# Kernel tuning notes

Hardware: AMD Instinct MI355X
Metric: run time of the kernel (lower is better)

The kernel has to match this reference:

```python
import jax, jax.numpy as jnp
import numpy as np

B, I, H = 4096, 1024, 2048
NUM_STEPS = 5
DT = 0.1

def setup_inputs() -> dict:
    key = jax.random.key(0)
    ks = jax.random.split(key, 5)
    # xavier-normal-ish scales for weights
    return {
        "x": jax.random.normal(ks[0], (B, I), jnp.float32),
        "hidden": jax.random.normal(ks[1], (B, H), jnp.float32),
        "W_rec": jax.random.normal(ks[2], (H, H), jnp.float32) * (2.0 / (H + H)) ** 0.5,
        "W_in_w": jax.random.normal(ks[3], (H, I), jnp.float32) * (2.0 / (I + H)) ** 0.5,
        "W_in_b": jnp.zeros((H,), jnp.float32),
        "tau_base": jnp.ones((H,), jnp.float32) * 2.0,
        "tau_adapt_w": jax.random.normal(ks[4], (H, I + H), jnp.float32) * (2.0 / (I + 2 * H)) ** 0.5,
        "tau_adapt_b": jnp.zeros((H,), jnp.float32),
    }

def reference(x, hidden, W_rec, W_in_w, W_in_b, tau_base, tau_adapt_w, tau_adapt_b):
    # x: [B, I], hidden: [B, H]
    input_contrib = x @ W_in_w.T + W_in_b          # loop-invariant: [B, H]
    x_tau = x @ tau_adapt_w[:, :I].T               # loop-invariant part of tau_adapt
    h = hidden
    tau = None
    for _ in range(NUM_STEPS):
        # tau_adapt(cat[x, h]) split into x-part + h-part (same math as concat matmul)
        tau_logits = x_tau + h @ tau_adapt_w[:, I:].T + tau_adapt_b
        tau = tau_base * (0.5 + jax.nn.sigmoid(tau_logits))   # [B, H]
        activated = jnp.tanh(h @ W_rec.T + input_contrib)     # [B, H]
        h = h + DT * (-h + activated) / tau
    return (h, tau)
```

## Files before the change

kernel.cpp:

```cpp
#include <hip/hip_runtime.h>
#include <hip/hip_bf16.h>

#define B_DIM 4096
#define I_DIM 1024
#define H_DIM 2048

typedef __attribute__((ext_vector_type(4))) float f32x4;
typedef __attribute__((ext_vector_type(8))) __bf16 bf16x8;

static __device__ __forceinline__ unsigned short f2bf(float f) {
  unsigned int u = __builtin_bit_cast(unsigned int, f);
  u += 0x7fffu + ((u >> 16) & 1u);
  return (unsigned short)(u >> 16);
}
static __device__ __forceinline__ float bf2f(unsigned short u) {
  unsigned int v = (unsigned int)u << 16;
  return __builtin_bit_cast(float, v);
}

__global__ void cvt_f32_bf16(const float* __restrict__ src,
                             unsigned short* __restrict__ dst,
                             int total4, int cols4, int src_ld4, int col04) {
  int t = blockIdx.x * blockDim.x + threadIdx.x;
  if (t >= total4) return;
  int row = t / cols4;
  int c = t - row * cols4;
  float4 v = reinterpret_cast<const float4*>(src)[(size_t)row * src_ld4 + col04 + c];
  ushort4 o;
  o.x = f2bf(v.x); o.y = f2bf(v.y); o.z = f2bf(v.z); o.w = f2bf(v.w);
  reinterpret_cast<ushort4*>(dst)[t] = o;
}

__global__ void cvt_ilv_bf16(const float* __restrict__ src,
                             unsigned short* __restrict__ dst,
                             int total4, int cols4, int src_ld4, int col04, int which) {
  int t = blockIdx.x * blockDim.x + threadIdx.x;
  if (t >= total4) return;
  int srow = t / cols4;
  int c = t - srow * cols4;
  int drow = ((srow >> 4) << 5) + (srow & 15) + which * 16;
  float4 v = reinterpret_cast<const float4*>(src)[(size_t)srow * src_ld4 + col04 + c];
  ushort4 o;
  o.x = f2bf(v.x); o.y = f2bf(v.y); o.z = f2bf(v.z); o.w = f2bf(v.w);
  reinterpret_cast<ushort4*>(dst)[(size_t)drow * cols4 + c] = o;
}

#define GLOAD_LDS16(gp, lp)                                                     \
  __builtin_amdgcn_global_load_lds(                                             \
      (const __attribute__((address_space(1))) void*)(gp),                      \
      (__attribute__((address_space(3))) void*)(lp), 16, 0, 0)

static __device__ __forceinline__ bf16x8 ldfrag(const unsigned short* p, int row, int l16) {
  return *reinterpret_cast<const bf16x8*>(p + row * 32 + ((l16 ^ ((row >> 1) & 3)) << 3));
}

template<int K, int MODE, bool WRITE_TAU>
__global__ __launch_bounds__(512, 2)
void gemm256(const unsigned short* __restrict__ Ab,
             const unsigned short* __restrict__ Wb,
             const unsigned short* __restrict__ add1b,
             const unsigned short* __restrict__ add2b,
             const float* __restrict__ wb,
             const float* __restrict__ tau_base,
             const float* __restrict__ tau_bias,
             const float* hprev,
             float* __restrict__ out1,
             float* out2,
             unsigned short* __restrict__ ob1,
             unsigned short* __restrict__ ob2) {
  __shared__ __align__(16) unsigned short lds[49152];

  const int tid  = threadIdx.x;
  const int lane = tid & 63;
  const int wid  = tid >> 6;
  const int wm   = wid >> 2;
  const int wn   = wid & 3;
  const int lr   = lane & 15;
  const int l16  = lane >> 4;

  const int bid = blockIdx.x;
  const int swz = (bid & 7) * 32 + (bid >> 3);
  const int bm = swz >> 4;
  const int bn = swz & 15;

  const unsigned short* Ag = Ab + (size_t)bm * 256 * K;
  const unsigned short* Wg = Wb + (size_t)bn * 256 * K;

  constexpr int NT = K / 32;

#define STAGE_OP(gcol, ldsbase)                                              \
  {                                                                          \
    { int s = tid;                                                           \
      int row = s >> 2;                                                      \
      int k16 = (s & 3) ^ ((row >> 1) & 3);                                  \
      GLOAD_LDS16((gcol) + (size_t)row * K + (k16 << 3),                     \
                  lds + (ldsbase) + s * 8); }                                \
    { int s = 512 + tid;                                                     \
      int row = s >> 2;                                                      \
      int k16 = (s & 3) ^ ((row >> 1) & 3);                                  \
      GLOAD_LDS16((gcol) + (size_t)row * K + (k16 << 3),                     \
                  lds + (ldsbase) + s * 8); }                                \
  }

  STAGE_OP(Ag, 0);
  STAGE_OP(Wg, 8192);
  STAGE_OP(Ag + 32, 16384);
  STAGE_OP(Wg + 32, 16384 + 8192);
  asm volatile("s_waitcnt vmcnt(4)" ::: "memory");
  __builtin_amdgcn_s_barrier();

  f32x4 acc[8][4];
  const f32x4 fz = {0.f, 0.f, 0.f, 0.f};
  #pragma unroll
  for (int i = 0; i < 8; ++i)
    #pragma unroll
    for (int j = 0; j < 4; ++j) acc[i][j] = fz;

  bf16x8 afr[4], bfr[4];
  int cb = 0;
  for (int t = 0; t < NT; ++t) {
    int nb = cb + 32768; if (nb >= 49152) nb -= 49152;
    const unsigned short* Acur = lds + cb;
    const unsigned short* Bcur = lds + cb + 8192;

    #pragma unroll
    for (int i = 0; i < 4; ++i) afr[i] = ldfrag(Acur, wm * 128 + i * 16 + lr, l16);
    #pragma unroll
    for (int j = 0; j < 4; ++j) bfr[j] = ldfrag(Bcur, wn * 64 + j * 16 + lr, l16);
    if (t + 2 < NT) { STAGE_OP(Ag + (size_t)(t + 2) * 32, nb); }
    asm volatile("" ::: "memory");
    __builtin_amdgcn_s_barrier();
    __builtin_amdgcn_s_setprio(1);
    #pragma unroll
    for (int i = 0; i < 4; ++i)
      #pragma unroll
      for (int j = 0; j < 4; ++j)
        acc[i][j] = __builtin_amdgcn_mfma_f32_16x16x32_bf16(afr[i], bfr[j], acc[i][j], 0, 0, 0);
    __builtin_amdgcn_s_setprio(0);
    __builtin_amdgcn_s_barrier();

    #pragma unroll
    for (int i = 0; i < 4; ++i) afr[i] = ldfrag(Acur, wm * 128 + (i + 4) * 16 + lr, l16);
    if (t + 2 < NT) { STAGE_OP(Wg + (size_t)(t + 2) * 32, nb + 8192); }
    asm volatile("" ::: "memory");
    if (t + 2 < NT)      { asm volatile("s_waitcnt vmcnt(4)" ::: "memory"); }
    else if (t + 1 < NT) { asm volatile("s_waitcnt vmcnt(0)" ::: "memory"); }
    __builtin_amdgcn_s_barrier();
    __builtin_amdgcn_s_setprio(1);
    #pragma unroll
    for (int i = 0; i < 4; ++i)
      #pragma unroll
      for (int j = 0; j < 4; ++j)
        acc[i + 4][j] = __builtin_amdgcn_mfma_f32_16x16x32_bf16(afr[i], bfr[j], acc[i + 4][j], 0, 0, 0);
    __builtin_amdgcn_s_setprio(0);
    __builtin_amdgcn_s_barrier();

    cb += 16384; if (cb >= 49152) cb = 0;
  }
#undef STAGE_OP

  const int rowg0 = bm * 256 + wm * 128 + l16 * 4;
  const int hcb = bn * 128 + wn * 32;
  #pragma unroll
  for (int p = 0; p < 2; ++p) {
    const int hc = hcb + p * 16 + lr;
    float tb = 0.f, tbi = 0.f, wbv = 0.f;
    if constexpr (MODE == 1) { tb = tau_base[hc]; tbi = tau_bias[hc]; }
    else                     { wbv = wb[hc]; }
    #pragma unroll
    for (int i = 0; i < 8; ++i) {
      const f32x4 c1 = acc[i][2 * p];
      const f32x4 c2 = acc[i][2 * p + 1];
      #pragma unroll
      for (int r = 0; r < 4; ++r) {
        const int row = rowg0 + i * 16 + r;
        const size_t idx = (size_t)row * H_DIM + hc;
        if constexpr (MODE == 0) {
          ob1[idx] = f2bf(c1[r] + wbv);
          ob2[idx] = f2bf(c2[r]);
        } else {
          const float hp  = hprev[idx];
          const float tl  = bf2f(add1b[idx]) + c1[r] + tbi;
          const float tau = tb * (0.5f + 1.f / (1.f + __expf(-tl)));
          const float pre = c2[r] + bf2f(add2b[idx]);
          const float act = 1.f - 2.f / (1.f + __expf(2.f * pre));
          const float hn  = hp + 0.1f * (act - hp) / tau;
          out1[idx] = hn;
          ob1[idx] = f2bf(hn);
          if constexpr (WRITE_TAU) out2[idx] = tau;
        }
      }
    }
  }
}

extern "C" void kernel_launch(void* const* d_in, const int* in_sizes, int n_in,
                              void* d_out, int out_size, void* d_ws, size_t ws_size,
                              hipStream_t stream) {
  const float* x           = (const float*)d_in[0];
  const float* hidden      = (const float*)d_in[1];
  const float* W_rec       = (const float*)d_in[2];
  const float* W_in_w      = (const float*)d_in[3];
  const float* W_in_b      = (const float*)d_in[4];
  const float* tau_base    = (const float*)d_in[5];
  const float* tau_adapt_w = (const float*)d_in[6];
  const float* tau_adapt_b = (const float*)d_in[7];

  float* out_h   = (float*)d_out;
  float* out_tau = (float*)d_out + (size_t)B_DIM * H_DIM;

  char* ws = (char*)d_ws;
  if (ws_size < 100663296u) return;
  unsigned short* x_bf   = (unsigned short*)(ws);
  unsigned short* hA_bf  = (unsigned short*)(ws +  8388608);
  unsigned short* hB_bf  = (unsigned short*)(ws + 25165824);
  unsigned short* Wpre   = (unsigned short*)(ws + 41943040);
  unsigned short* Wcat   = (unsigned short*)(ws + 50331648);
  unsigned short* icb    = (unsigned short*)(ws + 67108864);
  unsigned short* xtaub  = (unsigned short*)(ws + 83886080);

  cvt_f32_bf16<<<4096, 256, 0, stream>>>(x,      x_bf,  1048576, 256, 256, 0);
  cvt_f32_bf16<<<8192, 256, 0, stream>>>(hidden, hA_bf, 2097152, 512, 512, 0);
  cvt_ilv_bf16<<<2048, 256, 0, stream>>>(W_in_w,      Wpre, 524288, 256, 256, 0, 0);
  cvt_ilv_bf16<<<2048, 256, 0, stream>>>(tau_adapt_w, Wpre, 524288, 256, 768, 0, 1);
  cvt_ilv_bf16<<<4096, 256, 0, stream>>>(tau_adapt_w, Wcat, 1048576, 512, 768, 256, 0);
  cvt_ilv_bf16<<<4096, 256, 0, stream>>>(W_rec,       Wcat, 1048576, 512, 512, 0,   1);

  gemm256<1024, 0, false><<<256, 512, 0, stream>>>(
      x_bf, Wpre, nullptr, nullptr, W_in_b, nullptr, nullptr, nullptr,
      nullptr, nullptr, icb, xtaub);

  gemm256<2048, 1, false><<<256, 512, 0, stream>>>(
      hA_bf, Wcat, xtaub, icb, nullptr, tau_base, tau_adapt_b, hidden,
      out_h, nullptr, hB_bf, nullptr);
  gemm256<2048, 1, false><<<256, 512, 0, stream>>>(
      hB_bf, Wcat, xtaub, icb, nullptr, tau_base, tau_adapt_b, out_h,
      out_tau, nullptr, hA_bf, nullptr);
  gemm256<2048, 1, false><<<256, 512, 0, stream>>>(
      hA_bf, Wcat, xtaub, icb, nullptr, tau_base, tau_adapt_b, out_tau,
      out_h, nullptr, hB_bf, nullptr);
  gemm256<2048, 1, false><<<256, 512, 0, stream>>>(
      hB_bf, Wcat, xtaub, icb, nullptr, tau_base, tau_adapt_b, out_h,
      out_tau, nullptr, hA_bf, nullptr);
  gemm256<2048, 1, true><<<256, 512, 0, stream>>>(
      hA_bf, Wcat, xtaub, icb, nullptr, tau_base, tau_adapt_b, out_tau,
      out_h, out_tau, hB_bf, nullptr);
}
```

Baseline: 786.8 us.

## Shrink GEMM tile to 128x256 and launch 512 blocks for better CU fill

The GEMM tile shrinks from 256x256 to 128x256 rows per block. That halves the accumulator registers and the LDS footprint, raises the launch bound to 4 blocks per CU, and doubles the grid to 512 blocks so the 256 CUs are better filled. The k-loop is restructured to issue the A and B stage loads together with one barrier phase per k-step instead of two half-steps. The cost is lower arithmetic intensity per block and more re-reads of the weight tiles from L2.

```diff
diff --git a/kernel.cpp b/kernel.cpp
--- a/kernel.cpp
+++ b/kernel.cpp
@@ -55,20 +55,20 @@
 }
 
 template<int K, int MODE, bool WRITE_TAU>
-__global__ __launch_bounds__(512, 2)
-void gemm256(const unsigned short* __restrict__ Ab,
-             const unsigned short* __restrict__ Wb,
-             const unsigned short* __restrict__ add1b,
-             const unsigned short* __restrict__ add2b,
-             const float* __restrict__ wb,
-             const float* __restrict__ tau_base,
-             const float* __restrict__ tau_bias,
-             const float* hprev,
-             float* __restrict__ out1,
-             float* out2,
-             unsigned short* __restrict__ ob1,
-             unsigned short* __restrict__ ob2) {
-  __shared__ __align__(16) unsigned short lds[49152];
+__global__ __launch_bounds__(512, 4)
+void gemm128x256(const unsigned short* __restrict__ Ab,
+                 const unsigned short* __restrict__ Wb,
+                 const unsigned short* __restrict__ add1b,
+                 const unsigned short* __restrict__ add2b,
+                 const float* __restrict__ wb,
+                 const float* __restrict__ tau_base,
+                 const float* __restrict__ tau_bias,
+                 const float* hprev,
+                 float* __restrict__ out1,
+                 float* out2,
+                 unsigned short* __restrict__ ob1,
+                 unsigned short* __restrict__ ob2) {
+  __shared__ __align__(16) unsigned short lds[36864];
 
   const int tid  = threadIdx.x;
   const int lane = tid & 63;
@@ -79,57 +79,62 @@
   const int l16  = lane >> 4;
 
   const int bid = blockIdx.x;
-  const int swz = (bid & 7) * 32 + (bid >> 3);
-  const int bm = swz >> 4;
-  const int bn = swz & 15;
-
-  const unsigned short* Ag = Ab + (size_t)bm * 256 * K;
+  const int swz = (bid & 7) * 64 + (bid >> 3);
+  const int bn = swz >> 5;
+  const int bm = swz & 31;
+
+  const unsigned short* Ag = Ab + (size_t)bm * 128 * K;
   const unsigned short* Wg = Wb + (size_t)bn * 256 * K;
 
   constexpr int NT = K / 32;
 
-#define STAGE_OP(gcol, ldsbase)                                              \
-  {                                                                          \
-    { int s = tid;                                                           \
-      int row = s >> 2;                                                      \
+#define STAGE_A(gcol, base)                                                  \
+  { int s = tid; int row = s >> 2; int k16 = (s & 3) ^ ((row >> 1) & 3);     \
+    GLOAD_LDS16((gcol) + (size_t)row * K + (k16 << 3),                       \
+                lds + (base) + s * 8); }
+#define STAGE_B(gcol, base)                                                  \
+  { { int s = tid; int row = s >> 2; int k16 = (s & 3) ^ ((row >> 1) & 3);   \
+      GLOAD_LDS16((gcol) + (size_t)row * K + (k16 << 3),                     \
+                  lds + (base) + 4096 + s * 8); }                            \
+    { int s = 512 + tid; int row = s >> 2;                                   \
       int k16 = (s & 3) ^ ((row >> 1) & 3);                                  \
       GLOAD_LDS16((gcol) + (size_t)row * K + (k16 << 3),                     \
-                  lds + (ldsbase) + s * 8); }                                \
-    { int s = 512 + tid;                                                     \
-      int row = s >> 2;                                                      \
-      int k16 = (s & 3) ^ ((row >> 1) & 3);                                  \
-      GLOAD_LDS16((gcol) + (size_t)row * K + (k16 << 3),                     \
-                  lds + (ldsbase) + s * 8); }                                \
-  }
-
-  STAGE_OP(Ag, 0);
-  STAGE_OP(Wg, 8192);
-  STAGE_OP(Ag + 32, 16384);
-  STAGE_OP(Wg + 32, 16384 + 8192);
-  asm volatile("s_waitcnt vmcnt(4)" ::: "memory");
+                  lds + (base) + 4096 + s * 8); } }
+
+  STAGE_A(Ag, 0);
+  STAGE_B(Wg, 0);
+  STAGE_A(Ag + 32, 12288);
+  STAGE_B(Wg + 32, 12288);
+  asm volatile("s_waitcnt vmcnt(3)" ::: "memory");
   __builtin_amdgcn_s_barrier();
 
-  f32x4 acc[8][4];
+  f32x4 acc[4][4];
   const f32x4 fz = {0.f, 0.f, 0.f, 0.f};
   #pragma unroll
-  for (int i = 0; i < 8; ++i)
+  for (int i = 0; i < 4; ++i)
     #pragma unroll
     for (int j = 0; j < 4; ++j) acc[i][j] = fz;
 
-  bf16x8 afr[4], bfr[4];
   int cb = 0;
   for (int t = 0; t < NT; ++t) {
-    int nb = cb + 32768; if (nb >= 49152) nb -= 49152;
+    int nb = cb + 24576; if (nb >= 36864) nb -= 36864;
     const unsigned short* Acur = lds + cb;
-    const unsigned short* Bcur = lds + cb + 8192;
-
-    #pragma unroll
-    for (int i = 0; i < 4; ++i) afr[i] = ldfrag(Acur, wm * 128 + i * 16 + lr, l16);
+    const unsigned short* Bcur = lds + cb + 4096;
+
+    bf16x8 afr[4], bfr[4];
+    #pragma unroll
+    for (int i = 0; i < 4; ++i) afr[i] = ldfrag(Acur, wm * 64 + i * 16 + lr, l16);
     #pragma unroll
     for (int j = 0; j < 4; ++j) bfr[j] = ldfrag(Bcur, wn * 64 + j * 16 + lr, l16);
-    if (t + 2 < NT) { STAGE_OP(Ag + (size_t)(t + 2) * 32, nb); }
-    asm volatile("" ::: "memory");
-    __builtin_amdgcn_s_barrier();
+
+    if (t + 2 < NT) {
+      STAGE_A(Ag + (size_t)(t + 2) * 32, nb);
+      STAGE_B(Wg + (size_t)(t + 2) * 32, nb);
+      asm volatile("s_waitcnt vmcnt(3)" ::: "memory");
+    } else if (t + 1 < NT) {
+      asm volatile("s_waitcnt vmcnt(0)" ::: "memory");
+    }
+
     __builtin_amdgcn_s_setprio(1);
     #pragma unroll
     for (int i = 0; i < 4; ++i)
@@ -139,27 +144,12 @@
     __builtin_amdgcn_s_setprio(0);
     __builtin_amdgcn_s_barrier();
 
-    #pragma unroll
-    for (int i = 0; i < 4; ++i) afr[i] = ldfrag(Acur, wm * 128 + (i + 4) * 16 + lr, l16);
-    if (t + 2 < NT) { STAGE_OP(Wg + (size_t)(t + 2) * 32, nb + 8192); }
-    asm volatile("" ::: "memory");
-    if (t + 2 < NT)      { asm volatile("s_waitcnt vmcnt(4)" ::: "memory"); }
-    else if (t + 1 < NT) { asm volatile("s_waitcnt vmcnt(0)" ::: "memory"); }
-    __builtin_amdgcn_s_barrier();
-    __builtin_amdgcn_s_setprio(1);
-    #pragma unroll
-    for (int i = 0; i < 4; ++i)
-      #pragma unroll
-      for (int j = 0; j < 4; ++j)
-        acc[i + 4][j] = __builtin_amdgcn_mfma_f32_16x16x32_bf16(afr[i], bfr[j], acc[i + 4][j], 0, 0, 0);
-    __builtin_amdgcn_s_setprio(0);
-    __builtin_amdgcn_s_barrier();
-
-    cb += 16384; if (cb >= 49152) cb = 0;
+    cb += 12288; if (cb >= 36864) cb = 0;
   }
-#undef STAGE_OP
-
-  const int rowg0 = bm * 256 + wm * 128 + l16 * 4;
+#undef STAGE_A
+#undef STAGE_B
+
+  const int rowg0 = bm * 128 + wm * 64 + l16 * 4;
   const int hcb = bn * 128 + wn * 32;
   #pragma unroll
   for (int p = 0; p < 2; ++p) {
@@ -168,7 +158,7 @@
     if constexpr (MODE == 1) { tb = tau_base[hc]; tbi = tau_bias[hc]; }
     else                     { wbv = wb[hc]; }
     #pragma unroll
-    for (int i = 0; i < 8; ++i) {
+    for (int i = 0; i < 4; ++i) {
       const f32x4 c1 = acc[i][2 * p];
       const f32x4 c2 = acc[i][2 * p + 1];
       #pragma unroll
@@ -226,23 +216,23 @@
   cvt_ilv_bf16<<<4096, 256, 0, stream>>>(tau_adapt_w, Wcat, 1048576, 512, 768, 256, 0);
   cvt_ilv_bf16<<<4096, 256, 0, stream>>>(W_rec,       Wcat, 1048576, 512, 512, 0,   1);
 
-  gemm256<1024, 0, false><<<256, 512, 0, stream>>>(
+  gemm128x256<1024, 0, false><<<512, 512, 0, stream>>>(
       x_bf, Wpre, nullptr, nullptr, W_in_b, nullptr, nullptr, nullptr,
       nullptr, nullptr, icb, xtaub);
 
-  gemm256<2048, 1, false><<<256, 512, 0, stream>>>(
+  gemm128x256<2048, 1, false><<<512, 512, 0, stream>>>(
       hA_bf, Wcat, xtaub, icb, nullptr, tau_base, tau_adapt_b, hidden,
       out_h, nullptr, hB_bf, nullptr);
-  gemm256<2048, 1, false><<<256, 512, 0, stream>>>(
+  gemm128x256<2048, 1, false><<<512, 512, 0, stream>>>(
       hB_bf, Wcat, xtaub, icb, nullptr, tau_base, tau_adapt_b, out_h,
       out_tau, nullptr, hA_bf, nullptr);
-  gemm256<2048, 1, false><<<256, 512, 0, stream>>>(
+  gemm128x256<2048, 1, false><<<512, 512, 0, stream>>>(
       hA_bf, Wcat, xtaub, icb, nullptr, tau_base, tau_adapt_b, out_tau,
       out_h, nullptr, hB_bf, nullptr);
-  gemm256<2048, 1, false><<<256, 512, 0, stream>>>(
+  gemm128x256<2048, 1, false><<<512, 512, 0, stream>>>(
       hB_bf, Wcat, xtaub, icb, nullptr, tau_base, tau_adapt_b, out_h,
       out_tau, nullptr, hA_bf, nullptr);
-  gemm256<2048, 1, true><<<256, 512, 0, stream>>>(
+  gemm128x256<2048, 1, true><<<512, 512, 0, stream>>>(
       hA_bf, Wcat, xtaub, icb, nullptr, tau_base, tau_adapt_b, out_tau,
       out_h, out_tau, hB_bf, nullptr);
 }
```

After: 651.1 us. 17.2% less time.
